# Kernel optimization log

Hardware: AMD Instinct MI355X
Metric: run time of the kernel (lower is better)

The kernel has to match this reference:

```python
import jax, jax.numpy as jnp
import numpy as np

N_NODES = 10000
N_EDGES = 128000


def _edge_conv(x, row, col, edge_attr, w1, b1, w2, b2):
    # gather endpoints, concat edge features, 2-layer MLP per edge
    m = jnp.concatenate([x[row], x[col], edge_attr], axis=1)  # [E, 2*in+edge]
    m = jax.nn.relu(m @ w1 + b1) @ w2 + b2                    # [E, out]
    # scatter-mean onto source nodes (flow='target_to_source' -> aggregate on row)
    n = x.shape[0]
    s = jax.ops.segment_sum(m, row, num_segments=n)
    cnt = jax.ops.segment_sum(jnp.ones((row.shape[0], 1), m.dtype), row, num_segments=n)
    out = s / jnp.maximum(cnt, 1.0)
    return out, m


def setup_inputs() -> dict:
    key = jax.random.key(0)
    ks = jax.random.split(key, 24)
    f = jnp.float32

    def lin(kw, kb, fan_in, fan_out):
        lim = 1.0 / np.sqrt(fan_in)
        w = jax.random.uniform(kw, (fan_in, fan_out), f, -lim, lim)
        b = jax.random.uniform(kb, (fan_out,), f, -lim, lim)
        return w, b

    inp = {}
    inp['x_org'] = jax.random.normal(ks[0], (N_NODES, 256), f)
    inp['x_rot'] = jax.random.normal(ks[1], (N_NODES, 4), f)
    inp['edge_index'] = jax.random.randint(ks[2], (2, N_EDGES), 0, N_NODES, jnp.int64 if jax.config.jax_enable_x64 else jnp.int32)
    inp['edge_attr'] = jax.random.normal(ks[3], (N_EDGES, 640), f)
    inp['edge_rot'] = jax.random.normal(ks[4], (N_EDGES, 4), f)

    # conv1: Linear(2*260+644=1164, 64), Linear(64, 64)
    inp['c1_w1'], inp['c1_b1'] = lin(ks[5], ks[6], 1164, 64)
    inp['c1_w2'], inp['c1_b2'] = lin(ks[7], ks[8], 64, 64)
    # conv2: Linear(2*64+704=832, 64), Linear(64, 64)
    inp['c2_w1'], inp['c2_b1'] = lin(ks[9], ks[10], 832, 64)
    inp['c2_w2'], inp['c2_b2'] = lin(ks[11], ks[12], 64, 64)
    # conv3: Linear(2*128+128=384, 64), Linear(64, 64)
    inp['c3_w1'], inp['c3_b1'] = lin(ks[13], ks[14], 384, 64)
    inp['c3_w2'], inp['c3_b2'] = lin(ks[15], ks[16], 64, 64)
    # conv4: Linear(384, 64), Linear(64, 64)
    inp['c4_w1'], inp['c4_b1'] = lin(ks[17], ks[18], 384, 64)
    inp['c4_w2'], inp['c4_b2'] = lin(ks[19], ks[20], 64, 64)
    # lin1: Linear(64, 4)
    inp['lin1_w'], inp['lin1_b'] = lin(ks[21], ks[22], 64, 4)
    # edge_fc: Linear(64, 32) -> ReLU -> Linear(32, 1)
    k23 = jax.random.split(ks[23], 4)
    inp['efc_w1'], inp['efc_b1'] = lin(k23[0], k23[1], 64, 32)
    inp['efc_w2'], inp['efc_b2'] = lin(k23[2], k23[3], 32, 1)
    return inp


def reference(x_org, x_rot, edge_index, edge_attr, edge_rot,
              c1_w1, c1_b1, c1_w2, c1_b2,
              c2_w1, c2_b1, c2_w2, c2_b2,
              c3_w1, c3_b1, c3_w2, c3_b2,
              c4_w1, c4_b1, c4_w2, c4_b2,
              lin1_w, lin1_b, efc_w1, efc_b1, efc_w2, efc_b2):
    node_feat = jnp.concatenate([x_org, x_rot], axis=1)
    edge_feat = jnp.concatenate([edge_attr, edge_rot], axis=1)
    row, col = edge_index[0], edge_index[1]
    E = edge_index.shape[1]

    x1, edge_x1 = _edge_conv(node_feat, row, col, edge_feat, c1_w1, c1_b1, c1_w2, c1_b2)
    edge_x1 = jax.nn.relu(edge_x1)

    x2, edge_x2 = _edge_conv(x1, row, col, jnp.concatenate([edge_attr, edge_x1], axis=1),
                             c2_w1, c2_b1, c2_w2, c2_b2)
    x2 = jax.nn.relu(x2)
    edge_x2 = jax.nn.relu(edge_x2)

    x3, edge_x3 = _edge_conv(jnp.concatenate([x2, x1], axis=1), row, col,
                             jnp.concatenate([edge_x2, edge_x1], axis=1),
                             c3_w1, c3_b1, c3_w2, c3_b2)
    x3 = jax.nn.relu(x3)
    edge_x3 = jax.nn.relu(edge_x3)

    x4, edge_x4 = _edge_conv(jnp.concatenate([x3, x2], axis=1), row, col,
                             jnp.concatenate([edge_x3, edge_x2], axis=1),
                             c4_w1, c4_b1, c4_w2, c4_b2)
    x4 = jax.nn.relu(x4)

    x = x4 @ lin1_w + lin1_b  # [N, 4]
    h = edge_x4[: E // 2] + edge_x4[E // 2:]
    pred_edge_res = jax.nn.relu(h @ efc_w1 + efc_b1) @ efc_w2 + efc_b2  # [E/2, 1]

    # F.normalize(x, p=2, dim=1)
    x = x / jnp.maximum(jnp.linalg.norm(x, axis=1, keepdims=True), 1e-12)
    return x, pred_edge_res
```

## Files before the change

kernel.cpp:

```cpp
#include <hip/hip_runtime.h>
#include <stdint.h>


#define N_NODES 10000
#define N_EDGES 128000
#define E_HALF  64000
#define NBLK    1000

typedef unsigned short u16;

using bf16x8 = __attribute__((ext_vector_type(8))) short;
using f32x4  = __attribute__((ext_vector_type(4))) float;

#define MFMA16(A, B, C) C = __builtin_amdgcn_mfma_f32_16x16x32_bf16(A, B, C, 0, 0, 0)

__device__ __align__(256) float g_acc[N_NODES * 64];
__device__ __align__(256) float g_deg[N_NODES];
__device__ __align__(256) float g_P[N_NODES * 128];
__device__ __align__(256) float g_x1[N_NODES * 64];
__device__ __align__(256) float g_x2[N_NODES * 64];
__device__ __align__(256) float g_x3[N_NODES * 64];
__device__ __align__(256) u16  g_fragA[(size_t)NBLK * 16384];
__device__ __align__(256) u16  g_fragB[(size_t)NBLK * 16384];
__device__ __align__(256) float g_Q2 [(size_t)N_EDGES * 64];
__device__ __align__(256) float g_ex4[(size_t)N_EDGES * 64];
__device__ __align__(256) u16  g_wpA_hi[5 * 4096];
__device__ __align__(256) u16  g_wpA_lo[5 * 4096];
__device__ __align__(256) u16  g_wp2_hi[4 * 4096];
__device__ __align__(256) u16  g_wp2_lo[4 * 4096];
__device__ __align__(256) u16  g_wnp_hi[9 * 8192];
__device__ __align__(256) u16  g_wnp_lo[9 * 8192];
__device__ __align__(256) u16  g_wpC_hi[10 * 8192];
__device__ __align__(256) u16  g_wpC_lo[10 * 8192];
__device__ __align__(256) int g_row[N_EDGES];
__device__ __align__(256) int g_col[N_EDGES];
__device__ int g_mode;
__device__ int g_is64;

__device__ __forceinline__ float b2f(u16 u) {
    return __uint_as_float(((unsigned int)u) << 16);
}
__device__ __forceinline__ u16 f2b(float f) {
    unsigned int u = __float_as_uint(f);
    u += 0x7FFFu + ((u >> 16) & 1u);
    return (u16)(u >> 16);
}
__device__ __forceinline__ float ldf(const u16* p)   { return b2f(*p); }
__device__ __forceinline__ float ldf(const float* p) { return *p; }
__device__ __forceinline__ void  stf(u16* p, float v)   { *p = f2b(v); }
__device__ __forceinline__ void  stf(float* p, float v) { *p = v; }

__device__ __forceinline__ float4 load4(const float* p) { return *(const float4*)p; }
__device__ __forceinline__ float4 load4(const u16* p) {
    ushort4 v = *(const ushort4*)p;
    return make_float4(b2f(v.x), b2f(v.y), b2f(v.z), b2f(v.w));
}

__device__ __forceinline__ void gl_lds16(const void* g, void* l) {
    __builtin_amdgcn_global_load_lds(
        (const __attribute__((address_space(1))) void*)g,
        (__attribute__((address_space(3))) void*)l, 16, 0, 0);
}

__device__ __forceinline__ void split_pack(float4 v, uint2& hi, uint2& lo) {
    unsigned int ux = __float_as_uint(v.x), uy = __float_as_uint(v.y);
    unsigned int uz = __float_as_uint(v.z), uw = __float_as_uint(v.w);
    unsigned int hx = ux & 0xFFFF0000u, hy = uy & 0xFFFF0000u;
    unsigned int hz = uz & 0xFFFF0000u, hw = uw & 0xFFFF0000u;
    hi.x = (hx >> 16) | hy;
    hi.y = (hz >> 16) | hw;
    u16 lx = f2b(v.x - __uint_as_float(hx));
    u16 ly = f2b(v.y - __uint_as_float(hy));
    u16 lz = f2b(v.z - __uint_as_float(hz));
    u16 lw = f2b(v.w - __uint_as_float(hw));
    lo.x = (unsigned int)lx | ((unsigned int)ly << 16);
    lo.y = (unsigned int)lz | ((unsigned int)lw << 16);
}

__device__ __forceinline__ void mk_frag(float4 v0, float4 v1,
                                        bf16x8& fh, bf16x8& fl) {
    uint2 h0, l0, h1, l1;
    split_pack(v0, h0, l0);
    split_pack(v1, h1, l1);
    union { unsigned int w[4]; bf16x8 v; } H, L;
    H.w[0] = h0.x; H.w[1] = h0.y; H.w[2] = h1.x; H.w[3] = h1.y;
    L.w[0] = l0.x; L.w[1] = l0.y; L.w[2] = l1.x; L.w[3] = l1.y;
    fh = H.v; fl = L.v;
}

__global__ void prologue_a(const void* x_org_v, const int* __restrict__ eidx) {
    const int i = blockIdx.x * 256 + threadIdx.x;
    g_acc[i] = 0.f;
    if (i < N_NODES) g_deg[i] = 0.f;
    if (blockIdx.x == 0 && threadIdx.x < 64) {
        const u16* w = (const u16*)x_org_v;
        const int t = threadIdx.x;
        int ok = 0;
        for (int j = t; j < 128; j += 64) {
            u16 v = w[j];
            int ex = (v >> 7) & 0xFF;
            ok += ((ex >= 0x68 && ex <= 0x88) || ((v & 0x7FFFu) == 0)) ? 1 : 0;
        }
        #pragma unroll
        for (int off = 32; off >= 1; off >>= 1) ok += __shfl_xor(ok, off);
        bool allz = true;
        for (int j = t; j < 2048; j += 64) allz = allz && (eidx[2 * j + 1] == 0);
        unsigned long long m = __ballot(allz);
        if (t == 0) {
            g_mode = (ok >= 110) ? 0 : 1;
            g_is64 = (m == ~0ull) ? 1 : 0;
        }
    }
}

__device__ __forceinline__ void pack_pair(u16* dh, u16* dl, float v) {
    const u16 hh = f2b(v);
    *dh = hh; *dl = f2b(v - b2f(hh));
}
template<typename TW>
__device__ void pack_wnp(const TW* w, int hioff, int rem, u16* dh, u16* dl) {
    const int s = rem >> 13, kt = (rem >> 12) & 1, ct = (rem >> 9) & 7,
              l = (rem >> 3) & 63, r = rem & 7;
    const int k = s * 64 + kt * 32 + 4 * (l >> 4) + (r & 3) + 16 * (r >> 2);
    const int col = ct * 16 + (l & 15);
    const int row = (col < 64) ? k : (hioff + k);
    pack_pair(dh + rem, dl + rem, ldf(w + (size_t)row * 64 + (col & 63)));
}
template<typename TW>
__device__ void pack_wpa(const TW* w, int we, int rem, u16* dh, u16* dl) {
    const int s = rem >> 12, kt = (rem >> 11) & 1, ct = (rem >> 9) & 3,
              l = (rem >> 3) & 63, r = rem & 7;
    const int k = s * 64 + kt * 32 + 4 * (l >> 4) + (r & 3) + 16 * (r >> 2);
    pack_pair(dh + rem, dl + rem,
              ldf(w + (size_t)(we + k) * 64 + ct * 16 + (l & 15)));
}
template<typename TW>
__device__ void pack_wpc(const TW* w1, const TW* w2w, int rem) {
    const int s = rem >> 13, kt = (rem >> 12) & 1, ct = (rem >> 9) & 7,
              l = (rem >> 3) & 63, r = rem & 7;
    const int k = s * 64 + kt * 32 + 4 * (l >> 4) + (r & 3) + 16 * (r >> 2);
    const int col = ct * 16 + (l & 15);
    float v = (col < 64) ? ldf(w1 + (size_t)(520 + k) * 64 + col)
                         : ldf(w2w + (size_t)(128 + k) * 64 + (col - 64));
    pack_pair(g_wpC_hi + rem, g_wpC_lo + rem, v);
}

template<typename TW>
__device__ void pack_all_body(const TW* c1w1, const TW* c1w2, const TW* c2w1,
        const TW* c2w2, const TW* c3w1, const TW* c3w2, const TW* c4w1,
        const TW* c4w2) {
    const int idx = blockIdx.x * 256 + threadIdx.x;
    if (idx < 81920)        pack_wpc<TW>(c1w1, c2w1, idx);
    else if (idx < 114688)  pack_wnp<TW>(c1w1, 260, idx - 81920,  g_wnp_hi,            g_wnp_lo);
    else if (idx < 122880)  pack_wnp<TW>(c2w1, 64,  idx - 114688, g_wnp_hi + 4 * 8192, g_wnp_lo + 4 * 8192);
    else if (idx < 139264)  pack_wnp<TW>(c3w1, 128, idx - 122880, g_wnp_hi + 5 * 8192, g_wnp_lo + 5 * 8192);
    else if (idx < 155648)  pack_wnp<TW>(c4w1, 128, idx - 139264, g_wnp_hi + 7 * 8192, g_wnp_lo + 7 * 8192);
    else if (idx < 159744)  pack_wpa<TW>(c2w1, 768, idx - 155648, g_wpA_hi,            g_wpA_lo);
    else if (idx < 167936)  pack_wpa<TW>(c3w1, 256, idx - 159744, g_wpA_hi + 4096,     g_wpA_lo + 4096);
    else if (idx < 176128)  pack_wpa<TW>(c4w1, 256, idx - 167936, g_wpA_hi + 12288,    g_wpA_lo + 12288);
    else if (idx < 180224)  pack_wpa<TW>(c1w2, 0,   idx - 176128, g_wp2_hi,            g_wp2_lo);
    else if (idx < 184320)  pack_wpa<TW>(c2w2, 0,   idx - 180224, g_wp2_hi + 4096,     g_wp2_lo + 4096);
    else if (idx < 188416)  pack_wpa<TW>(c3w2, 0,   idx - 184320, g_wp2_hi + 8192,     g_wp2_lo + 8192);
    else if (idx < 192512)  pack_wpa<TW>(c4w2, 0,   idx - 188416, g_wp2_hi + 12288,    g_wp2_lo + 12288);
}

__global__ void prep_k(const void* c1w1, const void* c1w2, const void* c2w1,
        const void* c2w2, const void* c3w1, const void* c3w2, const void* c4w1,
        const void* c4w2, const int* __restrict__ eidx) {
    if ((int)blockIdx.x < 752) {
        if (g_mode == 0)
            pack_all_body<u16>((const u16*)c1w1, (const u16*)c1w2, (const u16*)c2w1,
                (const u16*)c2w2, (const u16*)c3w1, (const u16*)c3w2,
                (const u16*)c4w1, (const u16*)c4w2);
        else
            pack_all_body<float>((const float*)c1w1, (const float*)c1w2,
                (const float*)c2w1, (const float*)c2w2, (const float*)c3w1,
                (const float*)c3w2, (const float*)c4w1, (const float*)c4w2);
    } else {
        const int e = ((int)blockIdx.x - 752) * 256 + threadIdx.x;
        int row, col;
        if (g_is64) { row = eidx[2 * e]; col = eidx[2 * (e + N_EDGES)]; }
        else        { row = eidx[e];     col = eidx[e + N_EDGES]; }
        g_row[e] = row; g_col[e] = col;
        atomicAdd(&g_deg[row], 1.0f);
    }
}

template<typename TA>
__device__ void node_mfma_in_body(float* smrot, float* smwt,
        const TA* A1, const TA* rotsrc, const TA* w1, float* P) {
    const int t = threadIdx.x;
    const int lane = t & 63, wid = t >> 6;
    const int q = lane >> 4, n = lane & 15;
    const int r0b = blockIdx.x * 64;

    if (t < 64) {
        const int rr = min(r0b + t, N_NODES - 1);
        float4 v = load4(rotsrc + (size_t)rr * 4);
        smrot[t * 4 + 0] = v.x; smrot[t * 4 + 1] = v.y;
        smrot[t * 4 + 2] = v.z; smrot[t * 4 + 3] = v.w;
    }
    for (int i = t; i < 512; i += 256) {
        const int j = i >> 7, c = i & 127;
        const int row = (c < 64) ? (256 + j) : (516 + j);
        smwt[i] = ldf(w1 + (size_t)row * 64 + (c & 63));
    }
    __syncthreads();

    const int arow = min(r0b + wid * 16 + n, N_NODES - 1);

    f32x4 acc[8];
    #pragma unroll
    for (int ct = 0; ct < 8; ++ct) acc[ct] = (f32x4){0.f, 0.f, 0.f, 0.f};

    #pragma unroll
    for (int s = 0; s < 4; ++s) {
        #pragma unroll
        for (int kt = 0; kt < 2; ++kt) {
            const TA* p = A1 + (size_t)arow * 256 + s * 64 + kt * 32 + q * 4;
            float4 v0 = load4(p), v1 = load4(p + 16);
            bf16x8 ah, al;
            mk_frag(v0, v1, ah, al);
            const u16* wph = g_wnp_hi + s * 8192;
            const u16* wpl = g_wnp_lo + s * 8192;
            #pragma unroll
            for (int ct = 0; ct < 8; ++ct) {
                bf16x8 bh = *(const bf16x8*)&wph[(kt * 8 + ct) * 512 + lane * 8];
                bf16x8 bl = *(const bf16x8*)&wpl[(kt * 8 + ct) * 512 + lane * 8];
                MFMA16(ah, bh, acc[ct]);
                MFMA16(al, bh, acc[ct]);
                MFMA16(ah, bl, acc[ct]);
            }
        }
    }

    #pragma unroll
    for (int ct = 0; ct < 8; ++ct) {
        #pragma unroll
        for (int i = 0; i < 4; ++i) {
            const int rl = wid * 16 + 4 * q + i;
            const int row = r0b + rl;
            const int col = ct * 16 + n;
            float v = acc[ct][i]
                    + smrot[rl * 4 + 0] * smwt[0 * 128 + col]
                    + smrot[rl * 4 + 1] * smwt[1 * 128 + col]
                    + smrot[rl * 4 + 2] * smwt[2 * 128 + col]
                    + smrot[rl * 4 + 3] * smwt[3 * 128 + col];
            if (row < N_NODES) P[(size_t)row * 128 + col] = v;
        }
    }
}

__global__ void __launch_bounds__(256) node_mfma_in(
        const void* A1, const void* rotsrc, const void* w1, float* __restrict__ P) {
    __shared__ float smrot[256], smwt[512];
    if (g_mode == 0)
        node_mfma_in_body<u16>(smrot, smwt, (const u16*)A1, (const u16*)rotsrc,
                               (const u16*)w1, P);
    else
        node_mfma_in_body<float>(smrot, smwt, (const float*)A1, (const float*)rotsrc,
                               (const float*)w1, P);
}

template<int NS2, bool RELU>
__global__ void __launch_bounds__(256) node_mfma_acc(
        const float* A2, float* __restrict__ xout, float* __restrict__ P,
        int wnpoff) {
    const int t = threadIdx.x;
    const int lane = t & 63, wid = t >> 6;
    const int q = lane >> 4, n = lane & 15;
    const int r0b = blockIdx.x * 64;
    const int rown = r0b + wid * 16 + n;
    const int arow = min(rown, N_NODES - 1);
    const bool own = rown < N_NODES;
    const float inv = 1.0f / fmaxf(g_deg[arow], 1.0f);

    f32x4 acc[8];
    #pragma unroll
    for (int ct = 0; ct < 8; ++ct) acc[ct] = (f32x4){0.f, 0.f, 0.f, 0.f};

    #pragma unroll
    for (int kt = 0; kt < 2; ++kt) {
        float* p = g_acc + (size_t)arow * 64 + kt * 32 + q * 4;
        float4 v0 = load4(p), v1 = load4(p + 16);
        v0.x *= inv; v0.y *= inv; v0.z *= inv; v0.w *= inv;
        v1.x *= inv; v1.y *= inv; v1.z *= inv; v1.w *= inv;
        if (RELU) {
            v0.x = fmaxf(v0.x, 0.f); v0.y = fmaxf(v0.y, 0.f);
            v0.z = fmaxf(v0.z, 0.f); v0.w = fmaxf(v0.w, 0.f);
            v1.x = fmaxf(v1.x, 0.f); v1.y = fmaxf(v1.y, 0.f);
            v1.z = fmaxf(v1.z, 0.f); v1.w = fmaxf(v1.w, 0.f);
        }
        if (own) {
            *(float4*)(xout + (size_t)arow * 64 + kt * 32 + q * 4) = v0;
            *(float4*)(xout + (size_t)arow * 64 + kt * 32 + q * 4 + 16) = v1;
            *(float4*)p = make_float4(0.f, 0.f, 0.f, 0.f);
            *(float4*)(p + 16) = make_float4(0.f, 0.f, 0.f, 0.f);
        }
        bf16x8 ah, al;
        mk_frag(v0, v1, ah, al);
        const u16* wph = g_wnp_hi + wnpoff;
        const u16* wpl = g_wnp_lo + wnpoff;
        #pragma unroll
        for (int ct = 0; ct < 8; ++ct) {
            bf16x8 bh = *(const bf16x8*)&wph[(kt * 8 + ct) * 512 + lane * 8];
            bf16x8 bl = *(const bf16x8*)&wpl[(kt * 8 + ct) * 512 + lane * 8];
            MFMA16(ah, bh, acc[ct]);
            MFMA16(al, bh, acc[ct]);
            MFMA16(ah, bl, acc[ct]);
        }
    }
    if constexpr (NS2 > 0) {
        #pragma unroll
        for (int kt = 0; kt < 2; ++kt) {
            const float* p = A2 + (size_t)arow * 64 + kt * 32 + q * 4;
            float4 v0 = load4(p), v1 = load4(p + 16);
            bf16x8 ah, al;
            mk_frag(v0, v1, ah, al);
            const u16* wph = g_wnp_hi + wnpoff + 8192;
            const u16* wpl = g_wnp_lo + wnpoff + 8192;
            #pragma unroll
            for (int ct = 0; ct < 8; ++ct) {
                bf16x8 bh = *(const bf16x8*)&wph[(kt * 8 + ct) * 512 + lane * 8];
                bf16x8 bl = *(const bf16x8*)&wpl[(kt * 8 + ct) * 512 + lane * 8];
                MFMA16(ah, bh, acc[ct]);
                MFMA16(al, bh, acc[ct]);
                MFMA16(ah, bl, acc[ct]);
            }
        }
    }

    #pragma unroll
    for (int ct = 0; ct < 8; ++ct) {
        #pragma unroll
        for (int i = 0; i < 4; ++i) {
            const int rl = wid * 16 + 4 * q + i;
            const int row = r0b + rl;
            if (row < N_NODES) P[(size_t)row * 128 + ct * 16 + n] = acc[ct][i];
        }
    }
}

__device__ __forceinline__ void frag_store_o(u16* hreg, int wid, int lane,
        const f32x4 (&oacc)[2][4], u16* Fdst, int blkid) {
    const int q = lane >> 4, n = lane & 15;
    #pragma unroll
    for (int rt = 0; rt < 2; ++rt)
        #pragma unroll
        for (int ct = 0; ct < 4; ++ct)
            #pragma unroll
            for (int i = 0; i < 4; ++i) {
                float v = fmaxf(oacc[rt][ct][i], 0.f);
                unsigned int hb = __float_as_uint(v) & 0xFFFF0000u;
                const u16 hh = (u16)(hb >> 16);
                const u16 hl = f2b(v - __uint_as_float(hb));
                const int off = wid * 4096
                              + (((ct >> 1) * 2 + rt) * 64 + (n >> 2) * 16 + 4 * q + i) * 8
                              + (ct & 1) * 4 + (n & 3);
                hreg[off]        = hh;
                hreg[off + 2048] = hl;
            }
    #pragma unroll
    for (int kt = 0; kt < 2; ++kt)
        #pragma unroll
        for (int rtl = 0; rtl < 2; ++rtl) {
            const int src = wid * 4096 + ((kt * 2 + rtl) * 64 + lane) * 8;
            bf16x8 h8 = *(const bf16x8*)&hreg[src];
            bf16x8 l8 = *(const bf16x8*)&hreg[src + 2048];
            const size_t gb = (size_t)blkid * 16384
                            + (size_t)(kt * 8 + wid * 2 + rtl) * 512 + lane * 8;
            *(bf16x8*)&Fdst[gb]        = h8;
            *(bf16x8*)&Fdst[gb + 8192] = l8;
        }
}

template<typename TA, typename TW>
__device__ void edge_c1_body(u16* smW, int* srow, int* scol,
        float* b1s, float* b2s, float* rot, float* wtl,
        const TA* efa, const TA* rotsrc,
        const TW* w1, const TW* b1v, const TW* b2v) {
    const int t = threadIdx.x;
    const int lane = t & 63, wid = t >> 6;
    const int q = lane >> 4, n = lane & 15;
    const int e0 = blockIdx.x * 128;

    if (t < 128) srow[t] = g_row[e0 + t];
    else         scol[t - 128] = g_col[e0 + t - 128];
    if (t >= 128 && t < 192) b1s[t - 128] = ldf(b1v + (t - 128));
    if (t >= 192)            b2s[t - 192] = ldf(b2v + (t - 192));
    if (t < 128) {
        float4 r4 = load4(rotsrc + (size_t)(e0 + t) * 4);
        rot[t * 4 + 0] = r4.x; rot[t * 4 + 1] = r4.y;
        rot[t * 4 + 2] = r4.z; rot[t * 4 + 3] = r4.w;
    }
    wtl[t] = ldf(w1 + (size_t)(1160 + (t >> 6)) * 64 + (t & 63));

    const TA* arow0 = efa + (size_t)(e0 + wid * 32 + n) * 640;
    const TA* arow1 = efa + (size_t)(e0 + wid * 32 + 16 + n) * 640;

    f32x4 acc[2][8];
    #pragma unroll
    for (int a_ = 0; a_ < 2; ++a_)
        #pragma unroll
        for (int b_ = 0; b_ < 8; ++b_)
            acc[a_][b_] = (f32x4){0.f, 0.f, 0.f, 0.f};

    auto stageW = [&](int s) {
        const char* srch = (const char*)g_wpC_hi + (size_t)s * 16384;
        const char* srcl = (const char*)g_wpC_lo + (size_t)s * 16384;
        char* dsth = (char*)smW + (size_t)(s & 1) * 32768;
        char* dstl = dsth + 16384;
        #pragma unroll
        for (int i = 0; i < 4; ++i) {
            const int off = wid * 4096 + i * 1024;
            gl_lds16(srch + off + lane * 16, dsth + off);
            gl_lds16(srcl + off + lane * 16, dstl + off);
        }
    };
    auto stageW2 = [&]() {
        #pragma unroll
        for (int i = 0; i < 4; ++i) {
            const int L = wid * 4096 + i * 1024;
            const char* src = (L < 8192) ? (const char*)g_wp2_hi + L
                                         : (const char*)g_wp2_lo + (L - 8192);
            gl_lds16(src + lane * 16, (char*)smW + L);
        }
    };

    float4 abuf[3][2][2][2];
    auto issueA = [&](float4 (&buf)[2][2][2], int s) {
        const int cb = s * 64 + q * 4;
        #pragma unroll
        for (int kt = 0; kt < 2; ++kt) {
            buf[0][kt][0] = load4(arow0 + cb + kt * 32);
            buf[0][kt][1] = load4(arow0 + cb + kt * 32 + 16);
            buf[1][kt][0] = load4(arow1 + cb + kt * 32);
            buf[1][kt][1] = load4(arow1 + cb + kt * 32 + 16);
        }
    };
    auto step = [&](float4 (&buf)[2][2][2], int s) {
        const int wb = (s & 1) * 16384;
        #pragma unroll
        for (int kt = 0; kt < 2; ++kt) {
            bf16x8 ah0, al0, ah1, al1;
            mk_frag(buf[0][kt][0], buf[0][kt][1], ah0, al0);
            mk_frag(buf[1][kt][0], buf[1][kt][1], ah1, al1);
            #pragma unroll
            for (int ct = 0; ct < 8; ++ct) {
                bf16x8 bh = *(const bf16x8*)&smW[wb + (kt * 8 + ct) * 512 + lane * 8];
                bf16x8 bl = *(const bf16x8*)&smW[wb + 8192 + (kt * 8 + ct) * 512 + lane * 8];
                MFMA16(ah0, bh, acc[0][ct]);
                MFMA16(ah1, bh, acc[1][ct]);
                MFMA16(al0, bh, acc[0][ct]);
                MFMA16(al1, bh, acc[1][ct]);
                MFMA16(ah0, bl, acc[0][ct]);
                MFMA16(ah1, bl, acc[1][ct]);
            }
        }
    };

    stageW(0);
    issueA(abuf[0], 0);
    issueA(abuf[1], 1);
    __builtin_amdgcn_sched_barrier(0);
    asm volatile("s_waitcnt vmcnt(16) lgkmcnt(0)");
    __builtin_amdgcn_sched_barrier(0);
    __builtin_amdgcn_s_barrier();

    #pragma unroll
    for (int s = 0; s < 10; ++s) {
        if (s < 9) stageW(s + 1); else stageW2();
        __builtin_amdgcn_sched_barrier(0);
        if (s == 9) asm volatile("s_waitcnt vmcnt(4)");
        else        asm volatile("s_waitcnt vmcnt(16)");
        __builtin_amdgcn_sched_barrier(0);
        __builtin_amdgcn_s_barrier();
        if (s < 8) issueA(abuf[(s + 2) % 3], s + 2);
        step(abuf[s % 3], s);
        __builtin_amdgcn_s_barrier();
    }

    #pragma unroll
    for (int rt = 0; rt < 2; ++rt)
        #pragma unroll
        for (int c2 = 0; c2 < 4; ++c2)
            #pragma unroll
            for (int i = 0; i < 4; ++i) {
                const int rl = wid * 32 + rt * 16 + 4 * q + i;
                g_Q2[(size_t)(e0 + rl) * 64 + c2 * 16 + n] = acc[rt][4 + c2][i];
            }

    u16* hreg = smW + 16384;
    #pragma unroll
    for (int rt = 0; rt < 2; ++rt)
        #pragma unroll
        for (int ct = 0; ct < 4; ++ct)
            #pragma unroll
            for (int i = 0; i < 4; ++i) {
                const int rl = wid * 32 + rt * 16 + 4 * q + i;
                const int col = ct * 16 + n;
                float v = acc[rt][ct][i] + b1s[col]
                        + g_P[(size_t)srow[rl] * 128 + col]
                        + g_P[(size_t)scol[rl] * 128 + 64 + col]
                        + rot[rl * 4 + 0] * wtl[0 * 64 + col]
                        + rot[rl * 4 + 1] * wtl[1 * 64 + col]
                        + rot[rl * 4 + 2] * wtl[2 * 64 + col]
                        + rot[rl * 4 + 3] * wtl[3 * 64 + col];
                v = fmaxf(v, 0.f);
                unsigned int hb = __float_as_uint(v) & 0xFFFF0000u;
                const u16 hh = (u16)(hb >> 16);
                const u16 hl = f2b(v - __uint_as_float(hb));
                const int off = wid * 4096
                              + (((ct >> 1) * 2 + rt) * 64 + (n >> 2) * 16 + 4 * q + i) * 8
                              + (ct & 1) * 4 + (n & 3);
                hreg[off]        = hh;
                hreg[off + 2048] = hl;
            }

    __builtin_amdgcn_sched_barrier(0);
    asm volatile("s_waitcnt vmcnt(0)");
    __builtin_amdgcn_sched_barrier(0);
    __builtin_amdgcn_s_barrier();

    f32x4 oacc[2][4];
    #pragma unroll
    for (int rt = 0; rt < 2; ++rt)
        #pragma unroll
        for (int ct = 0; ct < 4; ++ct) {
            const float bb = b2s[ct * 16 + n];
            oacc[rt][ct] = (f32x4){bb, bb, bb, bb};
        }
    #pragma unroll
    for (int kt = 0; kt < 2; ++kt) {
        const int r0 = wid * 4096 + ((kt * 2 + 0) * 64 + lane) * 8;
        const int r1 = wid * 4096 + ((kt * 2 + 1) * 64 + lane) * 8;
        bf16x8 ah0 = *(const bf16x8*)&hreg[r0];
        bf16x8 ah1 = *(const bf16x8*)&hreg[r1];
        bf16x8 al0 = *(const bf16x8*)&hreg[r0 + 2048];
        bf16x8 al1 = *(const bf16x8*)&hreg[r1 + 2048];
        #pragma unroll
        for (int ct = 0; ct < 4; ++ct) {
            bf16x8 bh = *(const bf16x8*)&smW[(kt * 4 + ct) * 512 + lane * 8];
            bf16x8 bl = *(const bf16x8*)&smW[4096 + (kt * 4 + ct) * 512 + lane * 8];
            MFMA16(ah0, bh, oacc[0][ct]);
            MFMA16(ah1, bh, oacc[1][ct]);
            MFMA16(al0, bh, oacc[0][ct]);
            MFMA16(al1, bh, oacc[1][ct]);
            MFMA16(ah0, bl, oacc[0][ct]);
            MFMA16(ah1, bl, oacc[1][ct]);
        }
    }

    #pragma unroll
    for (int rt = 0; rt < 2; ++rt)
        #pragma unroll
        for (int ct = 0; ct < 4; ++ct)
            #pragma unroll
            for (int i = 0; i < 4; ++i) {
                const int rl = wid * 32 + rt * 16 + 4 * q + i;
                atomicAdd(&g_acc[(size_t)srow[rl] * 64 + ct * 16 + n], oacc[rt][ct][i]);
            }
    frag_store_o(hreg, wid, lane, oacc, g_fragA, blockIdx.x);
}

__global__ void __launch_bounds__(256, 2) edge_c1(
        const void* efa, const void* rotsrc,
        const void* w1, const void* b1, const void* b2) {
    __shared__ __align__(16) u16 smW[32768];
    __shared__ int srow[128], scol[128];
    __shared__ float b1s[64], b2s[64], rot[512], wtl[256];
    if (g_mode == 0)
        edge_c1_body<u16, u16>(smW, srow, scol, b1s, b2s, rot, wtl,
            (const u16*)efa, (const u16*)rotsrc,
            (const u16*)w1, (const u16*)b1, (const u16*)b2);
    else
        edge_c1_body<float, float>(smW, srow, scol, b1s, b2s, rot, wtl,
            (const float*)efa, (const float*)rotsrc,
            (const float*)w1, (const float*)b1, (const float*)b2);
}

template<typename TW, int NSF, bool HASQ2, bool FRAG_OUT>
__device__ void edge_lite_body(u16* smW, int* srow, int* scol,
        float* b1s, float* b2s,
        const u16* f0, const u16* f1,
        const TW* b1v, const TW* b2v, u16* Ffrag, float* fout,
        int wpAoff, int wp2off) {
    const int t = threadIdx.x;
    const int lane = t & 63, wid = t >> 6;
    const int q = lane >> 4, n = lane & 15;
    const int e0 = blockIdx.x * 128;
    const size_t blkb = (size_t)blockIdx.x * 16384;
    constexpr int N2 = 2 * NSF * 4096;

    #pragma unroll
    for (int i = 0; i < (NSF + 1) * 4; ++i) {
        const int L = wid * ((NSF + 1) * 4096) + i * 1024;
        const char* src;
        if (L < NSF * 8192)                 src = (const char*)(g_wpA_hi + wpAoff) + L;
        else if (L < 2 * NSF * 8192)        src = (const char*)(g_wpA_lo + wpAoff) + (L - NSF * 8192);
        else if (L < 2 * NSF * 8192 + 8192) src = (const char*)(g_wp2_hi + wp2off) + (L - 2 * NSF * 8192);
        else                                src = (const char*)(g_wp2_lo + wp2off) + (L - 2 * NSF * 8192 - 8192);
        gl_lds16(src + lane * 16, (char*)smW + L);
    }

    if (t < 128) srow[t] = g_row[e0 + t];
    else         scol[t - 128] = g_col[e0 + t - 128];
    if (t >= 128 && t < 192) b1s[t - 128] = ldf(b1v + (t - 128));
    if (t >= 192)            b2s[t - 192] = ldf(b2v + (t - 192));
    __syncthreads();

    f32x4 acc[2][4];
    #pragma unroll
    for (int a_ = 0; a_ < 2; ++a_)
        #pragma unroll
        for (int b_ = 0; b_ < 4; ++b_)
            acc[a_][b_] = (f32x4){0.f, 0.f, 0.f, 0.f};

    #pragma unroll
    for (int s = 0; s < NSF; ++s) {
        const u16* fs = (s == 0) ? f0 : f1;
        #pragma unroll
        for (int kt = 0; kt < 2; ++kt) {
            const size_t ba0 = blkb + (size_t)(kt * 8 + wid * 2 + 0) * 512 + lane * 8;
            const size_t ba1 = blkb + (size_t)(kt * 8 + wid * 2 + 1) * 512 + lane * 8;
            bf16x8 ah0 = *(const bf16x8*)&fs[ba0];
            bf16x8 al0 = *(const bf16x8*)&fs[ba0 + 8192];
            bf16x8 ah1 = *(const bf16x8*)&fs[ba1];
            bf16x8 al1 = *(const bf16x8*)&fs[ba1 + 8192];
            #pragma unroll
            for (int ct = 0; ct < 4; ++ct) {
                bf16x8 bh = *(const bf16x8*)&smW[s * 4096 + (kt * 4 + ct) * 512 + lane * 8];
                bf16x8 bl = *(const bf16x8*)&smW[NSF * 4096 + s * 4096 + (kt * 4 + ct) * 512 + lane * 8];
                MFMA16(ah0, bh, acc[0][ct]);
                MFMA16(ah1, bh, acc[1][ct]);
                MFMA16(al0, bh, acc[0][ct]);
                MFMA16(al1, bh, acc[1][ct]);
                MFMA16(ah0, bl, acc[0][ct]);
                MFMA16(ah1, bl, acc[1][ct]);
            }
        }
    }

    __builtin_amdgcn_s_barrier();
    u16* hreg = smW + (NSF == 1 ? 16384 : 0);

    #pragma unroll
    for (int rt = 0; rt < 2; ++rt)
        #pragma unroll
        for (int ct = 0; ct < 4; ++ct)
            #pragma unroll
            for (int i = 0; i < 4; ++i) {
                const int rl = wid * 32 + rt * 16 + 4 * q + i;
                const int col = ct * 16 + n;
                float v = acc[rt][ct][i] + b1s[col]
                        + g_P[(size_t)srow[rl] * 128 + col]
                        + g_P[(size_t)scol[rl] * 128 + 64 + col];
                if constexpr (HASQ2)
                    v += g_Q2[(size_t)(e0 + rl) * 64 + col];
                v = fmaxf(v, 0.f);
                unsigned int hb = __float_as_uint(v) & 0xFFFF0000u;
                const u16 hh = (u16)(hb >> 16);
                const u16 hl = f2b(v - __uint_as_float(hb));
                const int off = wid * 4096
                              + (((ct >> 1) * 2 + rt) * 64 + (n >> 2) * 16 + 4 * q + i) * 8
                              + (ct & 1) * 4 + (n & 3);
                hreg[off]        = hh;
                hreg[off + 2048] = hl;
            }

    f32x4 oacc[2][4];
    #pragma unroll
    for (int rt = 0; rt < 2; ++rt)
        #pragma unroll
        for (int ct = 0; ct < 4; ++ct) {
            const float bb = b2s[ct * 16 + n];
            oacc[rt][ct] = (f32x4){bb, bb, bb, bb};
        }
    #pragma unroll
    for (int kt = 0; kt < 2; ++kt) {
        const int r0 = wid * 4096 + ((kt * 2 + 0) * 64 + lane) * 8;
        const int r1 = wid * 4096 + ((kt * 2 + 1) * 64 + lane) * 8;
        bf16x8 ah0 = *(const bf16x8*)&hreg[r0];
        bf16x8 ah1 = *(const bf16x8*)&hreg[r1];
        bf16x8 al0 = *(const bf16x8*)&hreg[r0 + 2048];
        bf16x8 al1 = *(const bf16x8*)&hreg[r1 + 2048];
        #pragma unroll
        for (int ct = 0; ct < 4; ++ct) {
            bf16x8 bh = *(const bf16x8*)&smW[N2 + (kt * 4 + ct) * 512 + lane * 8];
            bf16x8 bl = *(const bf16x8*)&smW[N2 + 4096 + (kt * 4 + ct) * 512 + lane * 8];
            MFMA16(ah0, bh, oacc[0][ct]);
            MFMA16(ah1, bh, oacc[1][ct]);
            MFMA16(al0, bh, oacc[0][ct]);
            MFMA16(al1, bh, oacc[1][ct]);
            MFMA16(ah0, bl, oacc[0][ct]);
            MFMA16(ah1, bl, oacc[1][ct]);
        }
    }

    #pragma unroll
    for (int rt = 0; rt < 2; ++rt)
        #pragma unroll
        for (int ct = 0; ct < 4; ++ct)
            #pragma unroll
            for (int i = 0; i < 4; ++i) {
                const int rl = wid * 32 + rt * 16 + 4 * q + i;
                const int col = ct * 16 + n;
                const float v = oacc[rt][ct][i];
                atomicAdd(&g_acc[(size_t)srow[rl] * 64 + col], v);
                if constexpr (!FRAG_OUT)
                    fout[(size_t)(e0 + rl) * 64 + col] = v;
            }
    if constexpr (FRAG_OUT)
        frag_store_o(hreg, wid, lane, oacc, Ffrag, blockIdx.x);
}

template<int NSF, bool HASQ2, bool FRAG_OUT>
__global__ void __launch_bounds__(256, 2) edge_lite(
        const u16* f0, const u16* f1, const void* b1, const void* b2,
        u16* Ffrag, float* fout, int wpAoff, int wp2off) {
    __shared__ __align__(16) u16 smW[(NSF == 1) ? 32768 : 24576];
    __shared__ int srow[128], scol[128];
    __shared__ float b1s[64], b2s[64];
    if (g_mode == 0)
        edge_lite_body<u16, NSF, HASQ2, FRAG_OUT>(smW, srow, scol, b1s, b2s,
            f0, f1, (const u16*)b1, (const u16*)b2, Ffrag, fout, wpAoff, wp2off);
    else
        edge_lite_body<float, NSF, HASQ2, FRAG_OUT>(smW, srow, scol, b1s, b2s,
            f0, f1, (const float*)b1, (const float*)b2, Ffrag, fout, wpAoff, wp2off);
}

template<typename T>
__device__ void final_node_body(const T* w, const T* b, T* out, int bid) {
    const int t = threadIdx.x;
    const int lane = t & 63;
    const int n = bid * 4 + (t >> 6);
    float inv = 1.0f / fmaxf(g_deg[n], 1.0f);
    float x4 = fmaxf(g_acc[(size_t)n * 64 + lane] * inv, 0.0f);
    float r[4];
    #pragma unroll
    for (int j = 0; j < 4; ++j) {
        float v = x4 * ldf(w + lane * 4 + j);
        #pragma unroll
        for (int off = 32; off >= 1; off >>= 1) v += __shfl_xor(v, off);
        r[j] = v + ldf(b + j);
    }
    float nrm = sqrtf(r[0]*r[0] + r[1]*r[1] + r[2]*r[2] + r[3]*r[3]);
    float dn = fmaxf(nrm, 1e-12f);
    if (lane < 4) stf(out + n * 4 + lane, r[lane] / dn);
}

template<typename T>
__device__ void edge_head_body(const float* ex4, const T* w1, const T* b1,
                               const T* w2, const T* b2, T* out, int bid) {
    __shared__ float lw1[2048];
    __shared__ float lw2[32];
    const int t = threadIdx.x;
    for (int i = t; i < 2048; i += 256) lw1[i] = ldf(w1 + i);
    if (t < 32) lw2[t] = ldf(w2 + t);
    __syncthreads();
    const int e = bid * 256 + t;
    float a[32];
    #pragma unroll
    for (int j = 0; j < 32; ++j) a[j] = ldf(b1 + j);
    const float* p0 = ex4 + (size_t)e * 64;
    const float* p1 = ex4 + (size_t)(e + E_HALF) * 64;
    for (int c = 0; c < 64; ++c) {
        float h = p0[c] + p1[c];
        #pragma unroll
        for (int j = 0; j < 32; ++j) a[j] += h * lw1[c * 32 + j];
    }
    float s = ldf(b2);
    #pragma unroll
    for (int j = 0; j < 32; ++j) s += fmaxf(a[j], 0.f) * lw2[j];
    stf(out + e, s);
}

__global__ void __launch_bounds__(256) tail_k(
        const void* lw, const void* lb, const float* ex4,
        const void* ew1, const void* eb1, const void* ew2, const void* eb2,
        void* out) {
    const int b = blockIdx.x;
    if (b < 2500) {
        if (g_mode == 0) final_node_body<u16>((const u16*)lw, (const u16*)lb, (u16*)out, b);
        else             final_node_body<float>((const float*)lw, (const float*)lb, (float*)out, b);
    } else {
        if (g_mode == 0)
            edge_head_body<u16>(ex4, (const u16*)ew1, (const u16*)eb1,
                (const u16*)ew2, (const u16*)eb2, (u16*)out + 40000, b - 2500);
        else
            edge_head_body<float>(ex4, (const float*)ew1, (const float*)eb1,
                (const float*)ew2, (const float*)eb2, (float*)out + 40000, b - 2500);
    }
}

__global__ void sentinel_fill(unsigned int* out, int n_words) {
    int i = blockIdx.x * 256 + threadIdx.x;
    if (i < n_words) out[i] = 0x44794479u;
}

static void* sym_addr(const void* symbol) {
    void* p = nullptr;
    (void)hipGetSymbolAddress(&p, symbol);
    return p;
}

extern "C" void kernel_launch(void* const* d_in, const int* in_sizes, int n_in,
                              void* d_out, int out_size, void* d_ws, size_t ws_size,
                              hipStream_t stream) {
    (void)d_ws; (void)ws_size;
    bool ok = (n_in == 27) && (out_size == 104000)
           && (in_sizes[0] == 2560000) && (in_sizes[2] == 256000)
           && (in_sizes[3] == 81920000) && (in_sizes[5] == 74496)
           && (in_sizes[21] == 256) && (in_sizes[25] == 32);
    if (!ok) {
        sentinel_fill<<<204, 256, 0, stream>>>((unsigned int*)d_out, 52000);
        return;
    }
    const void* x_org     = d_in[0];
    const void* x_rot     = d_in[1];
    const int*  eidx      = (const int*)d_in[2];
    const void* edge_attr = d_in[3];
    const void* edge_rot  = d_in[4];

    float* P   = (float*)sym_addr(HIP_SYMBOL(g_P));
    float* x1  = (float*)sym_addr(HIP_SYMBOL(g_x1));
    float* x2  = (float*)sym_addr(HIP_SYMBOL(g_x2));
    float* x3  = (float*)sym_addr(HIP_SYMBOL(g_x3));
    u16*   fA  = (u16*)sym_addr(HIP_SYMBOL(g_fragA));
    u16*   fB  = (u16*)sym_addr(HIP_SYMBOL(g_fragB));
    float* ex4 = (float*)sym_addr(HIP_SYMBOL(g_ex4));

    prologue_a<<<2500, 256, 0, stream>>>(x_org, eidx);
    prep_k<<<1252, 256, 0, stream>>>(d_in[5], d_in[7], d_in[9], d_in[11],
                                     d_in[13], d_in[15], d_in[17], d_in[19], eidx);

    node_mfma_in<<<157, 256, 0, stream>>>(x_org, x_rot, d_in[5], P);
    edge_c1<<<NBLK, 256, 0, stream>>>(edge_attr, edge_rot, d_in[5], d_in[6], d_in[8]);

    node_mfma_acc<0, false><<<157, 256, 0, stream>>>(nullptr, x1, P, 4 * 8192);
    edge_lite<1, true, true><<<NBLK, 256, 0, stream>>>(
        fA, nullptr, d_in[10], d_in[12], fB, nullptr, 0, 4096);

    node_mfma_acc<1, true><<<157, 256, 0, stream>>>(x1, x2, P, 5 * 8192);
    edge_lite<2, false, true><<<NBLK, 256, 0, stream>>>(
        fB, fA, d_in[14], d_in[16], fA, nullptr, 4096, 8192);

    node_mfma_acc<1, true><<<157, 256, 0, stream>>>(x2, x3, P, 7 * 8192);
    edge_lite<2, false, false><<<NBLK, 256, 0, stream>>>(
        fA, fB, d_in[18], d_in[20], nullptr, ex4, 12288, 12288);

    tail_k<<<2750, 256, 0, stream>>>(d_in[21], d_in[22], ex4,
                                     d_in[23], d_in[24], d_in[25], d_in[26], d_out);
}
```

Before: 820.0 us.

## Store Q2 in per-thread fragment layout and shrink edge_lite LDS for occupancy

Q2 partial results are now written and read as contiguous per-thread float4 chunks in a block-local fragment layout, replacing strided scalar per-edge row accesses. The edge_lite LDS weight layout is repacked so the second-layer weights sit at a fixed offset and the hidden buffer reuses the first-layer weight region. This lets every variant use the smaller shared array, and launch bounds are raised to 3 blocks per CU. This reduces global memory transactions and raises occupancy, but the hidden-buffer aliasing relies on the barrier ordering, and the tighter launch bound may add register pressure.

After: 821.1 us. No clear change (+0.1%).

```diff
diff --git a/kernel.cpp b/kernel.cpp
--- a/kernel.cpp
+++ b/kernel.cpp
@@ -22,7 +22,7 @@
 __device__ __align__(256) float g_x3[N_NODES * 64];
 __device__ __align__(256) u16  g_fragA[(size_t)NBLK * 16384];
 __device__ __align__(256) u16  g_fragB[(size_t)NBLK * 16384];
-__device__ __align__(256) float g_Q2 [(size_t)N_EDGES * 64];
+__device__ __align__(256) float g_Q2 [(size_t)NBLK * 8192];
 __device__ __align__(256) float g_ex4[(size_t)N_EDGES * 64];
 __device__ __align__(256) u16  g_wpA_hi[5 * 4096];
 __device__ __align__(256) u16  g_wpA_lo[5 * 4096];
@@ -480,15 +480,14 @@
         __builtin_amdgcn_s_barrier();
     }
 
-    #pragma unroll
-    for (int rt = 0; rt < 2; ++rt)
-        #pragma unroll
-        for (int c2 = 0; c2 < 4; ++c2)
-            #pragma unroll
-            for (int i = 0; i < 4; ++i) {
-                const int rl = wid * 32 + rt * 16 + 4 * q + i;
-                g_Q2[(size_t)(e0 + rl) * 64 + c2 * 16 + n] = acc[rt][4 + c2][i];
-            }
+    {
+        float* qf = g_Q2 + (size_t)blockIdx.x * 8192 + (size_t)t * 32;
+        #pragma unroll
+        for (int rt = 0; rt < 2; ++rt)
+            #pragma unroll
+            for (int c2 = 0; c2 < 4; ++c2)
+                *(f32x4*)(qf + rt * 16 + c2 * 4) = acc[rt][4 + c2];
+    }
 
     u16* hreg = smW + 16384;
     #pragma unroll
@@ -590,17 +589,25 @@
     const int q = lane >> 4, n = lane & 15;
     const int e0 = blockIdx.x * 128;
     const size_t blkb = (size_t)blockIdx.x * 16384;
-    constexpr int N2 = 2 * NSF * 4096;
+    constexpr int N2 = 16384;
 
     #pragma unroll
     for (int i = 0; i < (NSF + 1) * 4; ++i) {
-        const int L = wid * ((NSF + 1) * 4096) + i * 1024;
+        const int j = i * 4 + wid;
         const char* src;
-        if (L < NSF * 8192)                 src = (const char*)(g_wpA_hi + wpAoff) + L;
-        else if (L < 2 * NSF * 8192)        src = (const char*)(g_wpA_lo + wpAoff) + (L - NSF * 8192);
-        else if (L < 2 * NSF * 8192 + 8192) src = (const char*)(g_wp2_hi + wp2off) + (L - 2 * NSF * 8192);
-        else                                src = (const char*)(g_wp2_lo + wp2off) + (L - 2 * NSF * 8192 - 8192);
-        gl_lds16(src + lane * 16, (char*)smW + L);
+        int dstB;
+        if (j < NSF * 8) {
+            src = (const char*)(g_wpA_hi + wpAoff) + j * 1024;            dstB = j * 1024;
+        } else if (j < NSF * 16) {
+            src = (const char*)(g_wpA_lo + wpAoff) + (j - NSF * 8) * 1024; dstB = j * 1024;
+        } else if (j < NSF * 16 + 8) {
+            src = (const char*)(g_wp2_hi + wp2off) + (j - NSF * 16) * 1024;
+            dstB = 32768 + (j - NSF * 16) * 1024;
+        } else {
+            src = (const char*)(g_wp2_lo + wp2off) + (j - NSF * 16 - 8) * 1024;
+            dstB = 32768 + (j - NSF * 16) * 1024;
+        }
+        gl_lds16(src + lane * 16, (char*)smW + dstB);
     }
 
     if (t < 128) srow[t] = g_row[e0 + t];
@@ -642,12 +649,15 @@
     }
 
     __builtin_amdgcn_s_barrier();
-    u16* hreg = smW + (NSF == 1 ? 16384 : 0);
-
+    u16* hreg = smW;
+
+    const float* qf = g_Q2 + (size_t)blockIdx.x * 8192 + (size_t)t * 32;
     #pragma unroll
     for (int rt = 0; rt < 2; ++rt)
         #pragma unroll
-        for (int ct = 0; ct < 4; ++ct)
+        for (int ct = 0; ct < 4; ++ct) {
+            f32x4 qv;
+            if constexpr (HASQ2) qv = *(const f32x4*)(qf + rt * 16 + ct * 4);
             #pragma unroll
             for (int i = 0; i < 4; ++i) {
                 const int rl = wid * 32 + rt * 16 + 4 * q + i;
@@ -655,8 +665,7 @@
                 float v = acc[rt][ct][i] + b1s[col]
                         + g_P[(size_t)srow[rl] * 128 + col]
                         + g_P[(size_t)scol[rl] * 128 + 64 + col];
-                if constexpr (HASQ2)
-                    v += g_Q2[(size_t)(e0 + rl) * 64 + col];
+                if constexpr (HASQ2) v += qv[i];
                 v = fmaxf(v, 0.f);
                 unsigned int hb = __float_as_uint(v) & 0xFFFF0000u;
                 const u16 hh = (u16)(hb >> 16);
@@ -667,6 +676,7 @@
                 hreg[off]        = hh;
                 hreg[off + 2048] = hl;
             }
+        }
 
     f32x4 oacc[2][4];
     #pragma unroll
@@ -715,10 +725,10 @@
 }
 
 template<int NSF, bool HASQ2, bool FRAG_OUT>
-__global__ void __launch_bounds__(256, 2) edge_lite(
+__global__ void __launch_bounds__(256, 3) edge_lite(
         const u16* f0, const u16* f1, const void* b1, const void* b2,
         u16* Ffrag, float* fout, int wpAoff, int wp2off) {
-    __shared__ __align__(16) u16 smW[(NSF == 1) ? 32768 : 24576];
+    __shared__ __align__(16) u16 smW[24576];
     __shared__ int srow[128], scol[128];
     __shared__ float b1s[64], b2s[64];
     if (g_mode == 0)
```
